# Performance work log

Measured on AMD Instinct MI355X. Metric: run time of the kernel, lower is better.

## Reference

```python
import jax, jax.numpy as jnp
import numpy as np

K0 = 16                       # partial-sum length used for the t-test
TAU = -2.053748910631823      # threshold from the kernel (negative -> test never passes)


def setup_inputs() -> dict:
    key = jax.random.key(0)
    kx, kw = jax.random.split(key)
    B, S, DIN, DOUT = 4, 2048, 4096, 4096
    x = jax.random.normal(kx, (B, S, DIN), dtype=jnp.float32)
    W = jax.random.normal(kw, (DOUT, DIN), dtype=jnp.float32) * 0.02
    return {"x": x, "W": W}


def reference(x, W):
    # Faithful translation of linear_etu_kernel (including its quirks):
    #  - phase 1: partial dot over first K0=16 features -> y1, s2
    #  - t-test: passed = |y1|/sqrt(s2/K0) < TAU (TAU<0 so always False)
    #  - phase 2: loops k in [K0, DOUT) but the loads omit the n/m offsets,
    #    so it accumulates a scalar c = sum_k W[0,k]*x_row0[k] into every
    #    still-active output. Bias is never read by the kernel.
    orig_shape = x.shape
    DOUT = W.shape[0]
    x2 = x.reshape(-1, orig_shape[-1])            # [N, DIN]
    xk = x2[:, :K0]                               # [N, K0]
    wk = W[:, :K0]                                # [DOUT, K0]
    y1 = xk @ wk.T                                # [N, DOUT]
    s2 = (xk * xk) @ (wk * wk).T                  # [N, DOUT] sum of prod^2
    tstat = jnp.abs(y1) / jnp.sqrt(s2 / K0)
    passed = tstat < TAU                          # always False (kept faithful)
    active = (~passed).astype(y1.dtype)
    # phase-2 quirk: uses W row 0 and x row 0 only, k in [K0, DOUT)
    c = jnp.sum(W[0, K0:DOUT] * x2[0, K0:DOUT])   # scalar
    acc = y1 + c * active
    out = jnp.where(passed, jnp.float32(0.0), acc)
    return out.reshape(*orig_shape[:-1], DOUT)
```

## Files before the change

### kernel.cpp

```cpp
#include <hip/hip_runtime.h>

constexpr int K0   = 16;
constexpr int DIN  = 4096;
constexpr int DOUT = 4096;

constexpr int BLOCK           = 256;
constexpr int COLS_PER_THREAD = 4;
constexpr int COLS_PER_BLOCK  = BLOCK * COLS_PER_THREAD;
constexpr int ROWS_PER_BLOCK  = 32;

typedef float vfloat4 __attribute__((ext_vector_type(4)));

__global__ __launch_bounds__(BLOCK) void et_fused(const float* __restrict__ x,
                                                  const float* __restrict__ W,
                                                  float* __restrict__ out) {
    __shared__ float lds_c[4];
    __shared__ float c_sh;
    const int tid  = threadIdx.x;
    const int j0   = blockIdx.x * COLS_PER_BLOCK + tid * COLS_PER_THREAD;
    const int row0 = blockIdx.y * ROWS_PER_BLOCK;

    float wk[COLS_PER_THREAD][K0];
    #pragma unroll
    for (int cc = 0; cc < COLS_PER_THREAD; ++cc) {
        const float4* wp = (const float4*)(W + (size_t)(j0 + cc) * DIN);
        #pragma unroll
        for (int q = 0; q < K0 / 4; ++q) {
            float4 v = wp[q];
            wk[cc][4 * q + 0] = v.x;
            wk[cc][4 * q + 1] = v.y;
            wk[cc][4 * q + 2] = v.z;
            wk[cc][4 * q + 3] = v.w;
        }
    }

    float acc = 0.0f;
    for (int t = K0 + tid; t < DIN; t += BLOCK)
        acc = fmaf(W[t], x[t], acc);
    #pragma unroll
    for (int off = 32; off > 0; off >>= 1)
        acc += __shfl_down(acc, off, 64);
    if ((tid & 63) == 0) lds_c[tid >> 6] = acc;
    __syncthreads();
    if (tid == 0) c_sh = lds_c[0] + lds_c[1] + lds_c[2] + lds_c[3];
    __syncthreads();
    const float c = c_sh;

    #pragma unroll 2
    for (int r = 0; r < ROWS_PER_BLOCK; ++r) {
        const int row = row0 + r;
        const float* xr = x + (size_t)row * DIN;

        float xk[K0];
        #pragma unroll
        for (int q = 0; q < K0 / 4; ++q) {
            float4 v = ((const float4*)xr)[q];
            xk[4 * q + 0] = v.x;
            xk[4 * q + 1] = v.y;
            xk[4 * q + 2] = v.z;
            xk[4 * q + 3] = v.w;
        }

        vfloat4 o;
        #pragma unroll
        for (int cc = 0; cc < COLS_PER_THREAD; ++cc) {
            float s = c;
            #pragma unroll
            for (int k = 0; k < K0; ++k)
                s = fmaf(xk[k], wk[cc][k], s);
            o[cc] = s;
        }
        __builtin_nontemporal_store(o, (vfloat4*)(out + (size_t)row * DOUT + j0));
    }
}

extern "C" void kernel_launch(void* const* d_in, const int* in_sizes, int n_in,
                              void* d_out, int out_size, void* d_ws, size_t ws_size,
                              hipStream_t stream) {
    const float* x = (const float*)d_in[0];
    const float* W = (const float*)d_in[1];
    float* out     = (float*)d_out;

    const int nrows = in_sizes[0] / DIN;

    dim3 grid(DOUT / COLS_PER_BLOCK, nrows / ROWS_PER_BLOCK);
    et_fused<<<grid, BLOCK, 0, stream>>>(x, W, out);
}
```

Before: 244.3 us.

## Stage x rows in LDS, vectorize scalar dot, halve rows per block

Each block now loads its rows' first 16 x features once into shared memory instead of every thread issuing the same global loads per row. The scalar phase-2 dot uses float4 loads. Rows per block drop from 32 to 16, which doubles the grid and repeats the scalar reduction and W-slice loads in twice as many blocks. Output stores switch from nontemporal to regular stores, which may change cache behaviour on a write-bound 128MB output.

```diff
diff --git a/kernel.cpp b/kernel.cpp
--- a/kernel.cpp
+++ b/kernel.cpp
@@ -4,25 +4,33 @@
 constexpr int DIN  = 4096;
 constexpr int DOUT = 4096;
 
-constexpr int BLOCK           = 256;
-constexpr int COLS_PER_THREAD = 4;
-constexpr int COLS_PER_BLOCK  = BLOCK * COLS_PER_THREAD;
-constexpr int ROWS_PER_BLOCK  = 32;
+constexpr int BLOCK          = 256;
+constexpr int CPT            = 4;
+constexpr int COLS_PER_BLOCK = BLOCK * CPT;
+constexpr int ROWS           = 16;
 
 typedef float vfloat4 __attribute__((ext_vector_type(4)));
 
 __global__ __launch_bounds__(BLOCK) void et_fused(const float* __restrict__ x,
                                                   const float* __restrict__ W,
                                                   float* __restrict__ out) {
+    __shared__ float xk_sh[ROWS][K0];
     __shared__ float lds_c[4];
     __shared__ float c_sh;
+
     const int tid  = threadIdx.x;
-    const int j0   = blockIdx.x * COLS_PER_BLOCK + tid * COLS_PER_THREAD;
-    const int row0 = blockIdx.y * ROWS_PER_BLOCK;
+    const int j0   = blockIdx.x * COLS_PER_BLOCK + tid * CPT;
+    const int row0 = blockIdx.y * ROWS;
 
-    float wk[COLS_PER_THREAD][K0];
+    float4 xs;
+    if (tid < ROWS * 4) {
+        const int r = tid >> 2, q = tid & 3;
+        xs = ((const float4*)(x + (size_t)(row0 + r) * DIN))[q];
+    }
+
+    float wk[CPT][K0];
     #pragma unroll
-    for (int cc = 0; cc < COLS_PER_THREAD; ++cc) {
+    for (int cc = 0; cc < CPT; ++cc) {
         const float4* wp = (const float4*)(W + (size_t)(j0 + cc) * DIN);
         #pragma unroll
         for (int q = 0; q < K0 / 4; ++q) {
@@ -34,43 +42,56 @@
         }
     }
 
-    float acc = 0.0f;
-    for (int t = K0 + tid; t < DIN; t += BLOCK)
-        acc = fmaf(W[t], x[t], acc);
-    #pragma unroll
-    for (int off = 32; off > 0; off >>= 1)
-        acc += __shfl_down(acc, off, 64);
-    if ((tid & 63) == 0) lds_c[tid >> 6] = acc;
+    {
+        const float4* xc = (const float4*)(x + K0);
+        const float4* wc = (const float4*)(W + K0);
+        float acc = 0.0f;
+        const int nq = (DIN - K0) / 4;
+        for (int t = tid; t < nq; t += BLOCK) {
+            float4 a = xc[t], b = wc[t];
+            acc = fmaf(a.x, b.x, acc);
+            acc = fmaf(a.y, b.y, acc);
+            acc = fmaf(a.z, b.z, acc);
+            acc = fmaf(a.w, b.w, acc);
+        }
+        #pragma unroll
+        for (int off = 32; off > 0; off >>= 1)
+            acc += __shfl_down(acc, off, 64);
+        if ((tid & 63) == 0) lds_c[tid >> 6] = acc;
+    }
+
+    if (tid < ROWS * 4) {
+        const int r = tid >> 2, q = tid & 3;
+        float* p = &xk_sh[r][4 * q];
+        p[0] = xs.x; p[1] = xs.y; p[2] = xs.z; p[3] = xs.w;
+    }
     __syncthreads();
     if (tid == 0) c_sh = lds_c[0] + lds_c[1] + lds_c[2] + lds_c[3];
     __syncthreads();
     const float c = c_sh;
 
-    #pragma unroll 2
-    for (int r = 0; r < ROWS_PER_BLOCK; ++r) {
-        const int row = row0 + r;
-        const float* xr = x + (size_t)row * DIN;
-
+    #pragma unroll 4
+    for (int r = 0; r < ROWS; ++r) {
         float xk[K0];
         #pragma unroll
         for (int q = 0; q < K0 / 4; ++q) {
-            float4 v = ((const float4*)xr)[q];
-            xk[4 * q + 0] = v.x;
-            xk[4 * q + 1] = v.y;
-            xk[4 * q + 2] = v.z;
-            xk[4 * q + 3] = v.w;
+            vfloat4 v = *((const vfloat4*)&xk_sh[r][4 * q]);
+            xk[4 * q + 0] = v[0];
+            xk[4 * q + 1] = v[1];
+            xk[4 * q + 2] = v[2];
+            xk[4 * q + 3] = v[3];
         }
 
         vfloat4 o;
         #pragma unroll
-        for (int cc = 0; cc < COLS_PER_THREAD; ++cc) {
+        for (int cc = 0; cc < CPT; ++cc) {
             float s = c;
             #pragma unroll
             for (int k = 0; k < K0; ++k)
                 s = fmaf(xk[k], wk[cc][k], s);
             o[cc] = s;
         }
-        __builtin_nontemporal_store(o, (vfloat4*)(out + (size_t)row * DOUT + j0));
+        *((vfloat4*)(out + (size_t)(row0 + r) * DOUT + j0)) = o;
     }
 }
 
@@ -83,6 +104,6 @@
 
     const int nrows = in_sizes[0] / DIN;
 
-    dim3 grid(DOUT / COLS_PER_BLOCK, nrows / ROWS_PER_BLOCK);
+    dim3 grid(DOUT / COLS_PER_BLOCK, nrows / ROWS);
     et_fused<<<grid, BLOCK, 0, stream>>>(x, W, out);
 }
```

New measurement: 232.8 us. 1.05x faster.
